# Optimization experiments

Hardware: AMD Instinct MI355X
Metric: run time of the kernel (lower is better)

Reference implementation:

```python
import jax, jax.numpy as jnp
import numpy as np

N_NODES = 50000
NEG_SLOPE = 0.2


def setup_inputs() -> dict:
    key = jax.random.key(0)
    k1, k2, k3, k4 = jax.random.split(key, 4)
    N, E, F, H, C = 50000, 800000, 128, 4, 32
    x = jax.random.normal(k1, (N, F), dtype=jnp.float32)
    edge_index = jax.random.randint(k2, (2, E), 0, N, dtype=jnp.int32)
    weight = jax.random.normal(k3, (F, H * C), dtype=jnp.float32) * 0.1  # glorot-ish scale
    att = jax.random.normal(k4, (1, H, 2 * C), dtype=jnp.float32) * 0.1
    bias = jnp.zeros((C,), dtype=jnp.float32)
    return {"x": x, "edge_index": edge_index, "weight": weight, "att": att, "bias": bias}


def reference(x, edge_index, weight, att, bias):
    N = x.shape[0]
    H, C2 = att.shape[1], att.shape[2]
    C = C2 // 2
    # linear projection -> [N, H, C]
    xw = jnp.matmul(x, weight).reshape(N, H, C)
    row, col = edge_index[0], edge_index[1]
    # per-edge attention logits: gather both endpoints, concat along channel
    x_i = xw[row]                     # [E, H, C]
    x_j = xw[col]                     # [E, H, C]
    cat_x = jnp.concatenate([x_i, x_j], axis=-1)      # [E, H, 2C]
    alpha = jnp.sum(cat_x * att, axis=-1)             # [E, H]
    alpha = jnp.where(alpha >= 0, alpha, NEG_SLOPE * alpha)  # leaky_relu
    # segment softmax grouped by row (source index, as in the torch code)
    seg_max = jax.ops.segment_max(alpha, row, num_segments=N)
    seg_max = jnp.where(jnp.isfinite(seg_max), seg_max, 0.0)
    alpha = jnp.exp(alpha - seg_max[row])
    seg_sum = jax.ops.segment_sum(alpha, row, num_segments=N)
    alpha = alpha / (seg_sum[row] + 1e-16)            # [E, H]
    # PyG propagate: message = alpha * x_j where x_j = x[edge_index[0]],
    # aggregated (scatter-add) into target = edge_index[1]
    msg = alpha[..., None] * xw[row]                  # [E, H, C]
    out = jax.ops.segment_sum(msg, col, num_segments=N)  # [N, H, C]
    out = out.mean(axis=1) + bias                     # concat=False -> head mean, + bias
    return out
```

## Files before the change

### kernel.cpp

```cpp
#include <hip/hip_runtime.h>
#include <hip/hip_fp16.h>

#define FDIM 128
#define HEADS 4
#define CD 32
#define BM 64
#define XPAD 68

static __device__ __forceinline__ unsigned short f2bf(float v) {
    unsigned u = __float_as_uint(v);
    u += 0x7FFF + ((u >> 16) & 1);
    return (unsigned short)(u >> 16);
}
static __device__ __forceinline__ float bf2f(unsigned short u) {
    return __uint_as_float(((unsigned)u) << 16);
}

__global__ __launch_bounds__(256) void k_gemm(const float* __restrict__ x,
                                              const float* __restrict__ w,
                                              const float* __restrict__ att,
                                              unsigned short* __restrict__ xwh,
                                              float* __restrict__ a_src,
                                              float* __restrict__ a_dst,
                                              float4* __restrict__ zero_base,
                                              int nz4, int N)
{
    __shared__ float xs[FDIM * XPAD];
    __shared__ float attl[HEADS * 2 * CD];
    int t = threadIdx.x;
    int row0 = blockIdx.x * BM;
    for (int i = blockIdx.x * 256 + t; i < nz4; i += gridDim.x * 256)
        zero_base[i] = make_float4(0.f, 0.f, 0.f, 0.f);
    attl[t] = att[t];
#pragma unroll
    for (int it = 0; it < 8; it++) {
        int i = t + 256 * it;
        int row = i & 63, kq = i >> 6;
        float4 v = make_float4(0.f, 0.f, 0.f, 0.f);
        if (row0 + row < N) v = ((const float4*)x)[(size_t)(row0 + row) * 32 + kq];
        xs[(kq * 4 + 0) * XPAD + row] = v.x;
        xs[(kq * 4 + 1) * XPAD + row] = v.y;
        xs[(kq * 4 + 2) * XPAD + row] = v.z;
        xs[(kq * 4 + 3) * XPAD + row] = v.w;
    }
    __syncthreads();
    int tx = t & 31, ty = t >> 5;
    int c0 = tx * 4, r0 = ty * 8;
    const float4* w4 = (const float4*)w;
    float acc[8][4];
#pragma unroll
    for (int i = 0; i < 8; i++)
#pragma unroll
        for (int j = 0; j < 4; j++) acc[i][j] = 0.f;
#pragma unroll 4
    for (int k = 0; k < FDIM; k++) {
        float4 wv = w4[k * 32 + tx];
        float4 xa = *(const float4*)&xs[k * XPAD + r0];
        float4 xb = *(const float4*)&xs[k * XPAD + r0 + 4];
        float xr[8] = {xa.x, xa.y, xa.z, xa.w, xb.x, xb.y, xb.z, xb.w};
        float wr[4] = {wv.x, wv.y, wv.z, wv.w};
#pragma unroll
        for (int i = 0; i < 8; i++)
#pragma unroll
            for (int j = 0; j < 4; j++) acc[i][j] += xr[i] * wr[j];
    }
    int h0 = c0 >> 5, chb = c0 & 31;
#pragma unroll
    for (int i = 0; i < 8; i++) {
        int r = row0 + r0 + i;
        if (r < N) {
#pragma unroll
            for (int j = 0; j < 4; j++)
                xwh[(size_t)r * FDIM + (chb + j) * 4 + h0] = f2bf(acc[i][j]);
        }
    }
    __syncthreads();
    float* accs = xs;
#pragma unroll
    for (int i = 0; i < 8; i++)
        *(float4*)&accs[(r0 + i) * 132 + c0] =
            make_float4(acc[i][0], acc[i][1], acc[i][2], acc[i][3]);
    __syncthreads();
    int row = t >> 2, h = t & 3;
    const float* ap = &attl[h * 2 * CD];
    const float* xr = &accs[row * 132 + h * CD];
    float s = 0.f, d = 0.f;
#pragma unroll 8
    for (int c = 0; c < CD; c++) { float v = xr[c]; s += v * ap[c]; d += v * ap[CD + c]; }
    int n = row0 + row;
    if (n < N) { a_src[n * 4 + h] = s; a_dst[n * 4 + h] = d; }
}

__global__ __launch_bounds__(256) void k_esum(const int* __restrict__ ei, int E,
                                              const float* __restrict__ a_src,
                                              const float* __restrict__ a_dst,
                                              float* __restrict__ seg,
                                              __half* __restrict__ ealpha)
{
    int gid = blockIdx.x * 256 + threadIdx.x;
    if (gid >= E * HEADS) return;
    int e = gid >> 2, h = gid & 3;
    int r = ei[e], cl = ei[E + e];
    float a = a_src[r * 4 + h] + a_dst[cl * 4 + h];
    a = a >= 0.f ? a : 0.2f * a;
    float ex = __expf(a);
    ealpha[gid] = __float2half(ex);
    atomicAdd(&seg[r * 4 + h], ex);
}

__global__ __launch_bounds__(256) void k_scatter(const int* __restrict__ ei, int E,
                                                 const __half* __restrict__ ealpha,
                                                 const float* __restrict__ seg,
                                                 const unsigned short* __restrict__ xwh,
                                                 __half2* __restrict__ out_acc2)
{
    int t = threadIdx.x;
    int le = t >> 4, c2 = t & 15;
    int e = blockIdx.x * 16 + le;
    if (e >= E) return;
    int r = ei[e], cl = ei[E + e];
    int lane = t & 63;
    float av = 0.f;
    if (c2 < 4) av = 0.25f * __half2float(ealpha[e * 4 + c2]) / (seg[r * 4 + c2] + 1e-16f);
    uint4 q = ((const uint4*)(xwh + (size_t)r * FDIM))[c2];
    float a0 = __shfl(av, (lane & 48) + 0, 64);
    float a1 = __shfl(av, (lane & 48) + 1, 64);
    float a2 = __shfl(av, (lane & 48) + 2, 64);
    float a3 = __shfl(av, (lane & 48) + 3, 64);
    float v0 = a0 * bf2f((unsigned short)(q.x & 0xFFFF)) + a1 * bf2f((unsigned short)(q.x >> 16))
             + a2 * bf2f((unsigned short)(q.y & 0xFFFF)) + a3 * bf2f((unsigned short)(q.y >> 16));
    float v1 = a0 * bf2f((unsigned short)(q.z & 0xFFFF)) + a1 * bf2f((unsigned short)(q.z >> 16))
             + a2 * bf2f((unsigned short)(q.w & 0xFFFF)) + a3 * bf2f((unsigned short)(q.w >> 16));
    unsafeAtomicAdd(&out_acc2[(size_t)cl * 16 + c2], __floats2half2_rn(v0, v1));
}

__global__ void k_final(const __half2* __restrict__ out_acc2, const float4* __restrict__ bias,
                        float4* __restrict__ out, int N)
{
    int i = blockIdx.x * 256 + threadIdx.x;
    if (i >= N * 8) return;
    float4 b = bias[i & 7];
    float2 f0 = __half22float2(out_acc2[i * 2]);
    float2 f1 = __half22float2(out_acc2[i * 2 + 1]);
    out[i] = make_float4(f0.x + b.x, f0.y + b.y, f1.x + b.z, f1.y + b.w);
}

extern "C" void kernel_launch(void* const* d_in, const int* in_sizes, int n_in,
                              void* d_out, int out_size, void* d_ws, size_t ws_size,
                              hipStream_t stream)
{
    const float* x    = (const float*)d_in[0];
    const int*   ei   = (const int*)d_in[1];
    const float* w    = (const float*)d_in[2];
    const float* att  = (const float*)d_in[3];
    const float* bias = (const float*)d_in[4];
    float* out = (float*)d_out;
    int N = in_sizes[0] / FDIM;
    int E = in_sizes[1] / 2;

    unsigned short* xwh = (unsigned short*)d_ws;
    float* fws      = (float*)(xwh + (size_t)N * FDIM);
    float* a_src    = fws;
    float* a_dst    = a_src + (size_t)N * HEADS;
    float* seg      = a_dst + (size_t)N * HEADS;
    __half2* out_acc2 = (__half2*)(seg + (size_t)N * HEADS);
    __half* ealpha  = (__half*)(out_acc2 + (size_t)N * 16);

    int nz4 = N * 5;

    k_gemm<<<(N + BM - 1) / BM, 256, 0, stream>>>(x, w, att, xwh, a_src, a_dst,
                                                  (float4*)seg, nz4, N);
    k_esum<<<(E * HEADS + 255) / 256, 256, 0, stream>>>(ei, E, a_src, a_dst, seg, ealpha);
    k_scatter<<<(E + 15) / 16, 256, 0, stream>>>(ei, E, ealpha, seg, xwh, out_acc2);
    k_final<<<(N * 8 + 255) / 256, 256, 0, stream>>>(out_acc2, (const float4*)bias, (float4*)out, N);
}
```

Measured before the change: 209.0 us.

## Run projection GEMM on bf16 MFMA with hi/lo split for fp32 accuracy

```diff
diff --git a/kernel.cpp b/kernel.cpp
--- a/kernel.cpp
+++ b/kernel.cpp
@@ -5,7 +5,9 @@
 #define HEADS 4
 #define CD 32
 #define BM 64
-#define XPAD 68
+
+typedef __attribute__((ext_vector_type(8))) short bfrag;
+typedef __attribute__((ext_vector_type(4))) float ffrag;
 
 static __device__ __forceinline__ unsigned short f2bf(float v) {
     unsigned u = __float_as_uint(v);
@@ -16,8 +18,22 @@
     return __uint_as_float(((unsigned)u) << 16);
 }
 
+__global__ __launch_bounds__(256) void k_wsplit(const float* __restrict__ w,
+                                                unsigned short* __restrict__ wt_hi,
+                                                unsigned short* __restrict__ wt_lo)
+{
+    int i = blockIdx.x * 256 + threadIdx.x;
+    float v = w[i];
+    unsigned short h = f2bf(v);
+    float r = v - bf2f(h);
+    int k = i >> 7, n = i & 127;
+    wt_hi[n * FDIM + k] = h;
+    wt_lo[n * FDIM + k] = f2bf(r);
+}
+
 __global__ __launch_bounds__(256) void k_gemm(const float* __restrict__ x,
-                                              const float* __restrict__ w,
+                                              const unsigned short* __restrict__ wt_hi,
+                                              const unsigned short* __restrict__ wt_lo,
                                               const float* __restrict__ att,
                                               unsigned short* __restrict__ xwh,
                                               float* __restrict__ a_src,
@@ -25,61 +41,67 @@
                                               float4* __restrict__ zero_base,
                                               int nz4, int N)
 {
-    __shared__ float xs[FDIM * XPAD];
+    __shared__ float accs[BM * 132];
     __shared__ float attl[HEADS * 2 * CD];
     int t = threadIdx.x;
     int row0 = blockIdx.x * BM;
     for (int i = blockIdx.x * 256 + t; i < nz4; i += gridDim.x * 256)
         zero_base[i] = make_float4(0.f, 0.f, 0.f, 0.f);
     attl[t] = att[t];
-#pragma unroll
-    for (int it = 0; it < 8; it++) {
-        int i = t + 256 * it;
-        int row = i & 63, kq = i >> 6;
-        float4 v = make_float4(0.f, 0.f, 0.f, 0.f);
-        if (row0 + row < N) v = ((const float4*)x)[(size_t)(row0 + row) * 32 + kq];
-        xs[(kq * 4 + 0) * XPAD + row] = v.x;
-        xs[(kq * 4 + 1) * XPAD + row] = v.y;
-        xs[(kq * 4 + 2) * XPAD + row] = v.z;
-        xs[(kq * 4 + 3) * XPAD + row] = v.w;
+
+    int l = t & 63, wv = t >> 6;
+    int la = l & 15, lr = l >> 4;
+    int arow = row0 + wv * 16 + la;
+    bool aval = arow < N;
+    const float* xbase = x + (size_t)arow * FDIM + lr * 8;
+
+    ffrag acc[8] = {};
+#pragma unroll
+    for (int ks = 0; ks < 4; ks++) {
+        float xv[8] = {0.f, 0.f, 0.f, 0.f, 0.f, 0.f, 0.f, 0.f};
+        if (aval) {
+            float4 f0 = *(const float4*)(xbase + ks * 32);
+            float4 f1 = *(const float4*)(xbase + ks * 32 + 4);
+            xv[0] = f0.x; xv[1] = f0.y; xv[2] = f0.z; xv[3] = f0.w;
+            xv[4] = f1.x; xv[5] = f1.y; xv[6] = f1.z; xv[7] = f1.w;
+        }
+        bfrag ah, al;
+#pragma unroll
+        for (int j = 0; j < 8; j++) {
+            unsigned short h = f2bf(xv[j]);
+            ah[j] = (short)h;
+            al[j] = (short)f2bf(xv[j] - bf2f(h));
+        }
+        int boff = ks * 32 + lr * 8;
+#pragma unroll
+        for (int ct = 0; ct < 8; ct++) {
+            int o = (ct * 16 + la) * FDIM + boff;
+            bfrag bh = *(const bfrag*)(wt_hi + o);
+            bfrag bl = *(const bfrag*)(wt_lo + o);
+            acc[ct] = __builtin_amdgcn_mfma_f32_16x16x32_bf16(ah, bh, acc[ct], 0, 0, 0);
+            acc[ct] = __builtin_amdgcn_mfma_f32_16x16x32_bf16(ah, bl, acc[ct], 0, 0, 0);
+            acc[ct] = __builtin_amdgcn_mfma_f32_16x16x32_bf16(al, bh, acc[ct], 0, 0, 0);
+        }
     }
-    __syncthreads();
-    int tx = t & 31, ty = t >> 5;
-    int c0 = tx * 4, r0 = ty * 8;
-    const float4* w4 = (const float4*)w;
-    float acc[8][4];
-#pragma unroll
-    for (int i = 0; i < 8; i++)
-#pragma unroll
-        for (int j = 0; j < 4; j++) acc[i][j] = 0.f;
-#pragma unroll 4
-    for (int k = 0; k < FDIM; k++) {
-        float4 wv = w4[k * 32 + tx];
-        float4 xa = *(const float4*)&xs[k * XPAD + r0];
-        float4 xb = *(const float4*)&xs[k * XPAD + r0 + 4];
-        float xr[8] = {xa.x, xa.y, xa.z, xa.w, xb.x, xb.y, xb.z, xb.w};
-        float wr[4] = {wv.x, wv.y, wv.z, wv.w};
-#pragma unroll
-        for (int i = 0; i < 8; i++)
-#pragma unroll
-            for (int j = 0; j < 4; j++) acc[i][j] += xr[i] * wr[j];
+
+#pragma unroll
+    for (int i = 0; i < 4; i++) {
+        int r = row0 + wv * 16 + lr * 4 + i;
+        if (r < N) {
+            uint2 pa, pb;
+            pa.x = (unsigned)f2bf(acc[0][i]) | ((unsigned)f2bf(acc[2][i]) << 16);
+            pa.y = (unsigned)f2bf(acc[4][i]) | ((unsigned)f2bf(acc[6][i]) << 16);
+            pb.x = (unsigned)f2bf(acc[1][i]) | ((unsigned)f2bf(acc[3][i]) << 16);
+            pb.y = (unsigned)f2bf(acc[5][i]) | ((unsigned)f2bf(acc[7][i]) << 16);
+            *(uint2*)&xwh[(size_t)r * FDIM + la * 4] = pa;
+            *(uint2*)&xwh[(size_t)r * FDIM + 64 + la * 4] = pb;
+        }
     }
-    int h0 = c0 >> 5, chb = c0 & 31;
-#pragma unroll
-    for (int i = 0; i < 8; i++) {
-        int r = row0 + r0 + i;
-        if (r < N) {
-#pragma unroll
-            for (int j = 0; j < 4; j++)
-                xwh[(size_t)r * FDIM + (chb + j) * 4 + h0] = f2bf(acc[i][j]);
-        }
-    }
-    __syncthreads();
-    float* accs = xs;
-#pragma unroll
-    for (int i = 0; i < 8; i++)
-        *(float4*)&accs[(r0 + i) * 132 + c0] =
-            make_float4(acc[i][0], acc[i][1], acc[i][2], acc[i][3]);
+#pragma unroll
+    for (int ct = 0; ct < 8; ct++)
+#pragma unroll
+        for (int i = 0; i < 4; i++)
+            accs[(wv * 16 + lr * 4 + i) * 132 + ct * 16 + la] = acc[ct][i];
     __syncthreads();
     int row = t >> 2, h = t & 3;
     const float* ap = &attl[h * 2 * CD];
@@ -165,10 +187,13 @@
     float* seg      = a_dst + (size_t)N * HEADS;
     __half2* out_acc2 = (__half2*)(seg + (size_t)N * HEADS);
     __half* ealpha  = (__half*)(out_acc2 + (size_t)N * 16);
+    unsigned short* wt_hi = (unsigned short*)(ealpha + (size_t)E * HEADS);
+    unsigned short* wt_lo = wt_hi + FDIM * FDIM;
 
     int nz4 = N * 5;
 
-    k_gemm<<<(N + BM - 1) / BM, 256, 0, stream>>>(x, w, att, xwh, a_src, a_dst,
+    k_wsplit<<<(FDIM * FDIM) / 256, 256, 0, stream>>>(w, wt_hi, wt_lo);
+    k_gemm<<<(N + BM - 1) / BM, 256, 0, stream>>>(x, wt_hi, wt_lo, att, xwh, a_src, a_dst,
                                                   (float4*)seg, nz4, N);
     k_esum<<<(E * HEADS + 255) / 256, 256, 0, stream>>>(ei, E, a_src, a_dst, seg, ealpha);
     k_scatter<<<(E + 15) / 16, 256, 0, stream>>>(ei, E, ealpha, seg, xwh, out_acc2);
```

Measured after the change: 210.0 us. About the same (+0.5%).
